# Kernel tuning notes

Hardware: AMD Instinct MI355X
Metric: run time of the kernel (lower is better)

The kernel has to match this reference:

```python
import jax, jax.numpy as jnp
import numpy as np
from jax import lax

B, C_IN, L = 512, 32, 512
E = 8
POOL = 16            # AdaptiveAvgPool1d(16)
D_IN = C_IN * L      # expert input = flattened x
D_OUT = 768          # pooler_output dim (hard-coded in module)
TAU = 1.0            # gumbel temperature
BN_EPS = 1e-5


def setup_inputs() -> dict:
    key = jax.random.key(0)
    ks = jax.random.split(key, 8)
    s = 0.02
    return {
        "x": jax.random.normal(ks[0], (B, C_IN, L), jnp.float32),
        "gumbel_u": jax.random.uniform(ks[1], (B, E), jnp.float32, 1e-6, 1.0 - 1e-6),
        "conv_w": jax.random.normal(ks[2], (64, C_IN, 3), jnp.float32) * s,
        "conv_b": jnp.zeros((64,), jnp.float32),
        "bn_gamma": jnp.ones((64 * POOL,), jnp.float32),
        "bn_beta": jnp.zeros((64 * POOL,), jnp.float32),
        "bn_mean": jnp.zeros((64 * POOL,), jnp.float32),
        "bn_var": jnp.ones((64 * POOL,), jnp.float32),
        "fc1_w": jax.random.normal(ks[3], (128, 64 * POOL), jnp.float32) * s,
        "fc1_b": jnp.zeros((128,), jnp.float32),
        "fc2_w": jax.random.normal(ks[4], (E, 128), jnp.float32) * s,
        "fc2_b": jnp.zeros((E,), jnp.float32),
        "expert_w": jax.random.normal(ks[5], (E, D_IN, D_OUT), jnp.float32) * s,
        "expert_b": jnp.zeros((E, D_OUT), jnp.float32),
    }


def _gelu(v):
    return jax.nn.gelu(v, approximate=False)  # torch nn.GELU default (erf)


def reference(x, gumbel_u, conv_w, conv_b, bn_gamma, bn_beta, bn_mean, bn_var,
              fc1_w, fc1_b, fc2_w, fc2_b, expert_w, expert_b):
    # ---- router ----
    h = lax.conv_general_dilated(x, conv_w, (1,), ((1, 1),),
                                 dimension_numbers=("NCH", "OIH", "NCH"))
    h = _gelu(h + conv_b[None, :, None])                     # [B,64,L]
    h = h.reshape(B, 64, POOL, L // POOL).mean(-1)           # adaptive avg pool -> [B,64,16]
    h = h.reshape(B, 64 * POOL)                              # flatten
    h = (h - bn_mean) * lax.rsqrt(bn_var + BN_EPS) * bn_gamma + bn_beta  # BN (eval)
    h = _gelu(h @ fc1_w.T + fc1_b)                           # dropout inactive in eval
    logits = h @ fc2_w.T + fc2_b                             # [B,E]

    # ---- soft gumbel-softmax gating (hard=False), then top-2 ----
    g = -jnp.log(-jnp.log(gumbel_u))
    routing_weights = jax.nn.softmax((logits + g) / TAU, axis=1)
    topv, topi = lax.top_k(routing_weights, 2)               # [B,2]
    w = topv / (topv.sum(axis=1, keepdims=True) + 1e-8)      # [B,2]

    # ---- dispatch/compute/combine (dense-expert stand-in: flatten + linear) ----
    xf = x.reshape(B, D_IN)
    all_out = jnp.einsum("bd,edh->beh", xf, expert_w) + expert_b[None]  # [B,E,768]
    sel = jnp.take_along_axis(all_out, topi[:, :, None], axis=1)        # [B,2,768]
    pooler_output = (sel * w[:, :, None]).sum(axis=1)                   # [B,768]
    return pooler_output
```

## Files before the change

### kernel.cpp

```cpp
#include <hip/hip_runtime.h>
#include <hip/hip_bf16.h>

#define NB 512
#define CIN 32
#define LEN 512
#define NE 8
#define NPOOL 16
#define DIN 16384
#define DOUT 768
#define HD 1024
#define F1 128

#define MT 256
#define NT 128
#define BK 32

typedef __attribute__((ext_vector_type(4))) float f32x4;
typedef __attribute__((ext_vector_type(8))) short s16x8;
typedef __attribute__((ext_vector_type(4))) unsigned int u32x4;

__device__ __forceinline__ float gelu_erf(float v) {
    return 0.5f * v * (1.0f + erff(v * 0.70710678118654752f));
}

__device__ __forceinline__ unsigned cvt_pk(float lo, float hi) {
    unsigned r;
    asm volatile("v_cvt_pk_bf16_f32 %0, %1, %2" : "=v"(r) : "v"(lo), "v"(hi));
    return r;
}

__device__ __forceinline__ unsigned short f2bf_u(float f) {
    union { float f; unsigned u; } x; x.f = f;
    unsigned r = x.u + 0x7fffu + ((x.u >> 16) & 1u);
    return (unsigned short)(r >> 16);
}

__device__ __forceinline__ void gload_lds16(const void* gptr, void* lptr) {
    __builtin_amdgcn_global_load_lds(
        (const __attribute__((address_space(1))) unsigned int*)gptr,
        (__attribute__((address_space(3))) unsigned int*)lptr,
        16, 0, 0);
}

__global__ __launch_bounds__(256) void krouter_conv(
    const float* __restrict__ x, const float* __restrict__ cw, const float* __restrict__ cb,
    const float* __restrict__ bng, const float* __restrict__ bnb,
    const float* __restrict__ bnm, const float* __restrict__ bnv,
    float* __restrict__ h, int* __restrict__ cnt, unsigned short* __restrict__ xbuf)
{
    __shared__ float xs[CIN * 264];
    int half = blockIdx.x;
    int b = blockIdx.y;
    int t = threadIdx.x;
    if (b == 0 && half == 0 && t < NE) cnt[t] = 0;

    int Lchunk0 = half * 64 - 1;
    const float* xb_ = x + (size_t)b * DIN;
    for (int idx = t; idx < CIN * 66; idx += 256) {
        int ci = idx / 66;
        int cc = idx - ci * 66;
        int gc = min(max(Lchunk0 + cc, 0), 127);
        f32x4 v = *(const f32x4*)(xb_ + ci * 512 + gc * 4);
        int byte = ci * 1056 + ((cc << 4) ^ (((cc >> 3) & 7) << 4));
        *(f32x4*)((char*)xs + byte) = v;
        if (cc >= 1 && cc <= 64) {
            int gc2 = Lchunk0 + cc;
            unsigned lo = cvt_pk(v[0], v[1]);
            unsigned hi = cvt_pk(v[2], v[3]);
            unsigned long long pk8 = ((unsigned long long)hi << 32) | lo;
            *(unsigned long long*)((char*)xbuf
                + ((size_t)b * DIN + ci * 512 + gc2 * 4) * 2) = pk8;
        }
    }
    __syncthreads();

    int p  = t & 7;
    int pg = half * 8 + p;
    int cq = t >> 3;
    int co0 = cq * 2, co1 = co0 + 1;

    float sa[32], sb[32];
    #pragma unroll
    for (int i = 0; i < 32; ++i) { sa[i] = 0.f; sb[i] = 0.f; }

    for (int ci = 0; ci < CIN; ++ci) {
        float f[40];
        #pragma unroll
        for (int u = 0; u < 10; ++u) {
            int lc = p * 8 + u;
            int byte = ci * 1056 + ((lc << 4) ^ (((lc >> 3) & 7) << 4));
            f32x4 v = *(const f32x4*)((const char*)xs + byte);
            f[4*u+0] = v[0]; f[4*u+1] = v[1]; f[4*u+2] = v[2]; f[4*u+3] = v[3];
        }
        if (pg == 0)  f[3]  = 0.f;
        if (pg == 15) f[36] = 0.f;
        float wa0 = cw[co0*96 + ci*3 + 0], wa1 = cw[co0*96 + ci*3 + 1], wa2 = cw[co0*96 + ci*3 + 2];
        float wb0 = cw[co1*96 + ci*3 + 0], wb1 = cw[co1*96 + ci*3 + 1], wb2 = cw[co1*96 + ci*3 + 2];
        #pragma unroll
        for (int i = 0; i < 32; ++i) {
            sa[i] = fmaf(f[i+3], wa0, fmaf(f[i+4], wa1, fmaf(f[i+5], wa2, sa[i])));
            sb[i] = fmaf(f[i+3], wb0, fmaf(f[i+4], wb1, fmaf(f[i+5], wb2, sb[i])));
        }
    }

    float ba = cb[co0], bbv = cb[co1];
    float ma = 0.f, mb = 0.f;
    #pragma unroll
    for (int i = 0; i < 32; ++i) { ma += gelu_erf(sa[i] + ba); mb += gelu_erf(sb[i] + bbv); }
    ma *= (1.f / 32.f); mb *= (1.f / 32.f);

    int oa = co0 * NPOOL + pg, ob = co1 * NPOOL + pg;
    float ra = (ma - bnm[oa]) * rsqrtf(bnv[oa] + 1e-5f) * bng[oa] + bnb[oa];
    float rb = (mb - bnm[ob]) * rsqrtf(bnv[ob] + 1e-5f) * bng[ob] + bnb[ob];
    h[(size_t)b * HD + oa] = ra;
    h[(size_t)b * HD + ob] = rb;
}

__global__ __launch_bounds__(256) void krouter_fc(
    const float* __restrict__ h, const float* __restrict__ f1w, const float* __restrict__ f1b,
    const float* __restrict__ f2w, const float* __restrict__ f2b,
    const float* __restrict__ gu,
    int* __restrict__ top2e, float* __restrict__ top2w,
    int* __restrict__ cnt, int* __restrict__ rowlist, float* __restrict__ roww)
{
    __shared__ float hs[4 * HD];
    __shared__ float h1s[4 * F1];
    __shared__ float lg[4 * NE];

    int bb = blockIdx.x * 4;
    int t = threadIdx.x;

    const f32x4* hg = (const f32x4*)(h + (size_t)bb * HD);
    f32x4* hs4 = (f32x4*)hs;
    #pragma unroll
    for (int u = 0; u < 4; ++u) hs4[t + 256 * u] = hg[t + 256 * u];
    __syncthreads();

    int j = t & 127;
    int pr = t >> 7;
    float acc[2] = {0.f, 0.f};
    const f32x4* w4 = (const f32x4*)(f1w + (size_t)j * HD);
    for (int k4 = 0; k4 < 256; ++k4) {
        f32x4 w = w4[k4];
        #pragma unroll
        for (int g = 0; g < 2; ++g) {
            f32x4 hv = hs4[(pr * 2 + g) * 256 + k4];
            acc[g] += w[0]*hv[0] + w[1]*hv[1] + w[2]*hv[2] + w[3]*hv[3];
        }
    }
    float bj = f1b[j];
    #pragma unroll
    for (int g = 0; g < 2; ++g) h1s[(pr * 2 + g) * F1 + j] = gelu_erf(acc[g] + bj);
    __syncthreads();

    if (t < 32) {
        int bi = t >> 3, e = t & 7;
        float s = f2b[e];
        const float* w = f2w + e * F1;
        const float* hh = h1s + bi * F1;
        #pragma unroll 8
        for (int k = 0; k < F1; ++k) s += hh[k] * w[k];
        lg[bi * NE + e] = s;
    }
    __syncthreads();

    if (t < 4) {
        int bi = t; int b = bb + bi;
        float r[NE];
        float mx = -1e30f;
        #pragma unroll
        for (int e = 0; e < NE; ++e) {
            float g = -logf(-logf(gu[b * NE + e]));
            r[e] = lg[bi * NE + e] + g;
            mx = fmaxf(mx, r[e]);
        }
        float sum = 0.f;
        #pragma unroll
        for (int e = 0; e < NE; ++e) { r[e] = expf(r[e] - mx); sum += r[e]; }
        float inv = 1.f / sum;
        #pragma unroll
        for (int e = 0; e < NE; ++e) r[e] *= inv;
        int e0 = 0; float v0 = r[0];
        #pragma unroll
        for (int e = 1; e < NE; ++e) if (r[e] > v0) { v0 = r[e]; e0 = e; }
        int e1 = -1; float v1 = -1.f;
        #pragma unroll
        for (int e = 0; e < NE; ++e) { if (e == e0) continue; if (r[e] > v1) { v1 = r[e]; e1 = e; } }
        float den = v0 + v1 + 1e-8f;
        float w0 = v0 / den, w1 = v1 / den;
        top2e[b * 2 + 0] = e0; top2e[b * 2 + 1] = e1;
        top2w[b * 2 + 0] = w0; top2w[b * 2 + 1] = w1;
        int p0 = atomicAdd(&cnt[e0], 1);
        rowlist[e0 * NB + p0] = b * 2 + 0; roww[e0 * NB + p0] = w0;
        int p1 = atomicAdd(&cnt[e1], 1);
        rowlist[e1 * NB + p1] = b * 2 + 1; roww[e1 * NB + p1] = w1;
    }
}

__global__ __launch_bounds__(512, 2) void kgemm(
    const unsigned short* __restrict__ xb, const float* __restrict__ ew,
    const int* __restrict__ cnt, const int* __restrict__ rowlist, const float* __restrict__ roww,
    unsigned short* __restrict__ ypart, int nkc, int kch)
{
    int nwg = gridDim.x;
    int cpx = nwg >> 3;
    int wg = (blockIdx.x & 7) * cpx + (blockIdx.x >> 3);
    int nt = wg % 6;
    int kc = (wg / 6) % nkc;
    int e  = wg / (6 * nkc);
    int cn = cnt[e];
    if (cn <= 0) return;

    __shared__ __align__(16) char As[3][MT * 64];
    __shared__ __align__(16) char Bs[2][NT * 64];

    int t = threadIdx.x;
    int wid = t >> 6, lane = t & 63;
    int wm = wid >> 1, wn = wid & 1;
    int g = lane >> 4;
    int NS = kch / BK;
    int k0 = kc * kch;

    int nl = t & 127, kg = t >> 7;
    const char* gpB = (const char*)ew + (size_t)e * DIN * DOUT * 4
                    + ((size_t)k0 + kg * 8) * (DOUT * 4) + (size_t)(nt * NT + nl) * 4;
    int swn = (nl ^ (nl >> 2)) & 3;
    int bwr_off = nl * 64 + ((kg ^ swn) << 4);

    int keya = ((lane >> 2) ^ (lane >> 4)) & 3;
    int aq = (lane & 3) ^ keya;
    int ldsA0 = wid * 2048, ldsA1 = wid * 2048 + 1024;

    int af_off[4], bf_off[4];
    #pragma unroll
    for (int mi = 0; mi < 4; ++mi) {
        int m = wm * 64 + mi * 16 + (lane & 15);
        af_off[mi] = m * 64 + ((g ^ ((m ^ (m >> 2)) & 3)) << 4);
    }
    #pragma unroll
    for (int ni = 0; ni < 4; ++ni) {
        int n = wn * 64 + ni * 16 + (lane & 15);
        bf_off[ni] = n * 64 + ((g ^ ((n ^ (n >> 2)) & 3)) << 4);
    }

    for (int row0 = 0; row0 < cn; row0 += MT) {
        int mloc = min(MT, cn - row0);
        bool wact = (wm * 64 < mloc);

        int r0 = wid * 32 + (lane >> 2);
        int r1 = r0 + 16;
        size_t ab0 = (size_t)(rowlist[e * NB + row0 + min(r0, mloc - 1)] >> 1) * ((size_t)DIN * 2);
        size_t ab1 = (size_t)(rowlist[e * NB + row0 + min(r1, mloc - 1)] >> 1) * ((size_t)DIN * 2);
        const char* gpA0 = (const char*)xb + ab0 + (size_t)k0 * 2 + (aq << 4);
        const char* gpA1 = (const char*)xb + ab1 + (size_t)k0 * 2 + (aq << 4);

        char* Acur = As[0]; char* Anx1 = As[1]; char* Anx2 = As[2];

        f32x4 acc[4][4];
        #pragma unroll
        for (int i = 0; i < 4; ++i)
            #pragma unroll
            for (int jj = 0; jj < 4; ++jj) acc[i][jj] = (f32x4){0.f, 0.f, 0.f, 0.f};

        float Bq0[8], Bq1[8];

        gload_lds16(gpA0, Acur + ldsA0);
        gload_lds16(gpA1, Acur + ldsA1);
        #pragma unroll
        for (int j = 0; j < 8; ++j) Bq0[j] = *(const float*)(gpB + j * (DOUT * 4));
        gload_lds16(gpA0 + BK * 2, Anx1 + ldsA0);
        gload_lds16(gpA1 + BK * 2, Anx1 + ldsA1);
        #pragma unroll
        for (int j = 0; j < 8; ++j)
            Bq1[j] = *(const float*)(gpB + (size_t)(BK * DOUT * 4) + j * (DOUT * 4));
        __builtin_amdgcn_sched_barrier(0);
        asm volatile("s_waitcnt vmcnt(10)" ::: "memory");
        __builtin_amdgcn_sched_barrier(0);
        {
            u32x4 pk;
            pk[0] = cvt_pk(Bq0[0], Bq0[1]); pk[1] = cvt_pk(Bq0[2], Bq0[3]);
            pk[2] = cvt_pk(Bq0[4], Bq0[5]); pk[3] = cvt_pk(Bq0[6], Bq0[7]);
            *(u32x4*)(Bs[0] + bwr_off) = pk;
        }
        asm volatile("s_waitcnt lgkmcnt(0)" ::: "memory");
        __builtin_amdgcn_sched_barrier(0);
        __builtin_amdgcn_s_barrier();
        __builtin_amdgcn_sched_barrier(0);

#define GSTEP(S, BLD, BCV)                                                        \
        {                                                                         \
            int s_ = (S);                                                         \
            if (s_ + 2 < NS) {                                                    \
                size_t ao = (size_t)(s_ + 2) * (BK * 2);                          \
                gload_lds16(gpA0 + ao, Anx2 + ldsA0);                             \
                gload_lds16(gpA1 + ao, Anx2 + ldsA1);                             \
                const char* bsrc = gpB + (size_t)(s_ + 2) * ((size_t)BK * DOUT * 4); \
                _Pragma("unroll")                                                 \
                for (int j = 0; j < 8; ++j)                                       \
                    BLD[j] = *(const float*)(bsrc + j * (DOUT * 4));              \
            }                                                                     \
            __builtin_amdgcn_sched_barrier(0);                                    \
            if (wact) {                                                           \
                const char* Bb = Bs[s_ & 1];                                      \
                __builtin_amdgcn_s_setprio(1);                                    \
                s16x8 af[4];                                                      \
                _Pragma("unroll")                                                 \
                for (int mi = 0; mi < 4; ++mi)                                    \
                    af[mi] = *(const s16x8*)(Acur + af_off[mi]);                  \
                _Pragma("unroll")                                                 \
                for (int ni = 0; ni < 4; ++ni) {                                  \
                    s16x8 bf = *(const s16x8*)(Bb + bf_off[ni]);                  \
                    _Pragma("unroll")                                             \
                    for (int mi = 0; mi < 4; ++mi)                                \
                        acc[mi][ni] = __builtin_amdgcn_mfma_f32_16x16x32_bf16(    \
                            af[mi], bf, acc[mi][ni], 0, 0, 0);                    \
                }                                                                 \
                __builtin_amdgcn_s_setprio(0);                                    \
            }                                                                     \
            __builtin_amdgcn_sched_barrier(0);                                    \
            if (s_ + 2 < NS)      asm volatile("s_waitcnt vmcnt(10)" ::: "memory"); \
            else if (s_ + 1 < NS) asm volatile("s_waitcnt vmcnt(0)" ::: "memory"); \
            __builtin_amdgcn_sched_barrier(0);                                    \
            if (s_ + 1 < NS) {                                                    \
                u32x4 pk;                                                         \
                pk[0] = cvt_pk(BCV[0], BCV[1]); pk[1] = cvt_pk(BCV[2], BCV[3]);   \
                pk[2] = cvt_pk(BCV[4], BCV[5]); pk[3] = cvt_pk(BCV[6], BCV[7]);   \
                *(u32x4*)(Bs[(s_ + 1) & 1] + bwr_off) = pk;                       \
            }                                                                     \
            asm volatile("s_waitcnt lgkmcnt(0)" ::: "memory");                    \
            __builtin_amdgcn_sched_barrier(0);                                    \
            __builtin_amdgcn_s_barrier();                                         \
            __builtin_amdgcn_sched_barrier(0);                                    \
            { char* tmp_ = Acur; Acur = Anx1; Anx1 = Anx2; Anx2 = tmp_; }         \
        }

        for (int s = 0; s < NS; s += 2) {
            GSTEP(s, Bq0, Bq1);
            GSTEP(s + 1, Bq1, Bq0);
        }
#undef GSTEP

        if (wact) {
            #pragma unroll
            for (int mi = 0; mi < 4; ++mi) {
                #pragma unroll
                for (int rg = 0; rg < 4; ++rg) {
                    int m = wm * 64 + mi * 16 + g * 4 + rg;
                    if (m < mloc) {
                        int ent = rowlist[e * NB + row0 + m];
                        float wgt = roww[e * NB + row0 + m];
                        int ob = ent >> 1, slot = ent & 1;
                        unsigned short* dst = ypart + ((size_t)(slot * nkc + kc) * NB + ob) * DOUT
                                            + nt * NT + wn * 64 + (lane & 15);
                        #pragma unroll
                        for (int ni = 0; ni < 4; ++ni)
                            dst[ni * 16] = f2bf_u(acc[mi][ni][rg] * wgt);
                    }
                }
            }
        }
        asm volatile("s_waitcnt vmcnt(0) lgkmcnt(0)" ::: "memory");
        __builtin_amdgcn_s_barrier();
    }
}

__global__ __launch_bounds__(256) void kcombine(
    const unsigned short* __restrict__ ypart,
    const int* __restrict__ top2e, const float* __restrict__ top2w,
    const float* __restrict__ eb, float* __restrict__ out, int nplanes)
{
    int b = blockIdx.y;
    int n = blockIdx.x * 256 + threadIdx.x;
    float s = 0.f;
    for (int p = 0; p < nplanes; ++p) {
        unsigned v = ypart[((size_t)p * NB + b) * DOUT + n];
        union { unsigned u; float f; } c; c.u = v << 16;
        s += c.f;
    }
    int e0 = top2e[b * 2], e1 = top2e[b * 2 + 1];
    float w0 = top2w[b * 2], w1 = top2w[b * 2 + 1];
    s += w0 * eb[e0 * DOUT + n] + w1 * eb[e1 * DOUT + n];
    out[(size_t)b * DOUT + n] = s;
}

extern "C" void kernel_launch(void* const* d_in, const int* in_sizes, int n_in,
                              void* d_out, int out_size, void* d_ws, size_t ws_size,
                              hipStream_t stream)
{
    const float* x   = (const float*)d_in[0];
    const float* gu  = (const float*)d_in[1];
    const float* cw  = (const float*)d_in[2];
    const float* cb  = (const float*)d_in[3];
    const float* bng = (const float*)d_in[4];
    const float* bnb = (const float*)d_in[5];
    const float* bnm = (const float*)d_in[6];
    const float* bnv = (const float*)d_in[7];
    const float* f1w = (const float*)d_in[8];
    const float* f1b = (const float*)d_in[9];
    const float* f2w = (const float*)d_in[10];
    const float* f2b = (const float*)d_in[11];
    const float* ew  = (const float*)d_in[12];
    const float* eb  = (const float*)d_in[13];

    int nkc = (ws_size >= (size_t)48 * 1024 * 1024) ? 16 : 8;
    int kch = DIN / nkc;

    char* ws = (char*)d_ws;
    size_t off = 0;
    float* h       = (float*)(ws + off); off += (size_t)NB * HD * 4;
    int*   top2e   = (int*)(ws + off);   off += (size_t)NB * 2 * 4;
    float* top2w   = (float*)(ws + off); off += (size_t)NB * 2 * 4;
    int*   cnt     = (int*)(ws + off);   off += 256;
    int*   rowlist = (int*)(ws + off);   off += (size_t)NE * NB * 4;
    float* roww    = (float*)(ws + off); off += (size_t)NE * NB * 4;
    unsigned short* xbuf = (unsigned short*)(ws + off);
    off += (size_t)NB * DIN * 2;
    unsigned short* ypart = (unsigned short*)(ws + off);
    off += (size_t)2 * nkc * NB * DOUT * 2;

    krouter_conv<<<dim3(2, NB), 256, 0, stream>>>(x, cw, cb, bng, bnb, bnm, bnv, h, cnt, xbuf);
    krouter_fc<<<NB / 4, 256, 0, stream>>>(h, f1w, f1b, f2w, f2b, gu,
                                           top2e, top2w, cnt, rowlist, roww);
    kgemm<<<NE * nkc * 6, 512, 0, stream>>>(xbuf, ew, cnt, rowlist, roww, ypart, nkc, kch);
    kcombine<<<dim3(3, NB), 256, 0, stream>>>(ypart, top2e, top2w, eb, (float*)d_out, 2 * nkc);
}
```

Measured before the change: 265.8 us.

## Replace LDS-staged expert GEMM with register-direct MFMA strips per wave

The grouped expert GEMM no longer stages A and B tiles through shared memory with barriers. Each wave now owns a 32-column output strip and loads A fragments (gathered token rows) and fp32 B weights straight into registers, converts B to bf16 in registers and issues MFMAs over 160-row M chunks with double-buffered register prefetch. The workgroup shrinks to 256 threads and the K split is fixed at 16. This removes LDS traffic and barrier synchronisation, but A rows are re-read from global memory by every strip and register pressure rises with 10 M fragments.

After: 337.1 us. 26.8% more time.

```diff
diff --git a/kernel.cpp b/kernel.cpp
--- a/kernel.cpp
+++ b/kernel.cpp
@@ -11,9 +11,10 @@
 #define HD 1024
 #define F1 128
 
-#define MT 256
-#define NT 128
 #define BK 32
+#define MFR 10
+#define KSPLIT 16
+#define NSTRIP 24
 
 typedef __attribute__((ext_vector_type(4))) float f32x4;
 typedef __attribute__((ext_vector_type(8))) short s16x8;
@@ -33,13 +34,6 @@
     union { float f; unsigned u; } x; x.f = f;
     unsigned r = x.u + 0x7fffu + ((x.u >> 16) & 1u);
     return (unsigned short)(r >> 16);
-}
-
-__device__ __forceinline__ void gload_lds16(const void* gptr, void* lptr) {
-    __builtin_amdgcn_global_load_lds(
-        (const __attribute__((address_space(1))) unsigned int*)gptr,
-        (__attribute__((address_space(3))) unsigned int*)lptr,
-        16, 0, 0);
 }
 
 __global__ __launch_bounds__(256) void krouter_conv(
@@ -197,171 +191,107 @@
     }
 }
 
-__global__ __launch_bounds__(512, 2) void kgemm(
+__global__ __launch_bounds__(256, 2) void kgemm(
     const unsigned short* __restrict__ xb, const float* __restrict__ ew,
     const int* __restrict__ cnt, const int* __restrict__ rowlist, const float* __restrict__ roww,
-    unsigned short* __restrict__ ypart, int nkc, int kch)
+    unsigned short* __restrict__ ypart, int kch)
 {
     int nwg = gridDim.x;
     int cpx = nwg >> 3;
     int wg = (blockIdx.x & 7) * cpx + (blockIdx.x >> 3);
-    int nt = wg % 6;
-    int kc = (wg / 6) % nkc;
-    int e  = wg / (6 * nkc);
-    int cn = cnt[e];
-    if (cn <= 0) return;
-
-    __shared__ __align__(16) char As[3][MT * 64];
-    __shared__ __align__(16) char Bs[2][NT * 64];
+    int e  = wg / (KSPLIT * 6);
+    int r  = wg % (KSPLIT * 6);
+    int kc = r / 6;
+    int bg = r % 6;
 
     int t = threadIdx.x;
     int wid = t >> 6, lane = t & 63;
-    int wm = wid >> 1, wn = wid & 1;
+    int st = bg * 4 + wid;
     int g = lane >> 4;
+    int cn = cnt[e];
     int NS = kch / BK;
     int k0 = kc * kch;
 
-    int nl = t & 127, kg = t >> 7;
     const char* gpB = (const char*)ew + (size_t)e * DIN * DOUT * 4
-                    + ((size_t)k0 + kg * 8) * (DOUT * 4) + (size_t)(nt * NT + nl) * 4;
-    int swn = (nl ^ (nl >> 2)) & 3;
-    int bwr_off = nl * 64 + ((kg ^ swn) << 4);
-
-    int keya = ((lane >> 2) ^ (lane >> 4)) & 3;
-    int aq = (lane & 3) ^ keya;
-    int ldsA0 = wid * 2048, ldsA1 = wid * 2048 + 1024;
-
-    int af_off[4], bf_off[4];
-    #pragma unroll
-    for (int mi = 0; mi < 4; ++mi) {
-        int m = wm * 64 + mi * 16 + (lane & 15);
-        af_off[mi] = m * 64 + ((g ^ ((m ^ (m >> 2)) & 3)) << 4);
-    }
-    #pragma unroll
-    for (int ni = 0; ni < 4; ++ni) {
-        int n = wn * 64 + ni * 16 + (lane & 15);
-        bf_off[ni] = n * 64 + ((g ^ ((n ^ (n >> 2)) & 3)) << 4);
-    }
-
-    for (int row0 = 0; row0 < cn; row0 += MT) {
-        int mloc = min(MT, cn - row0);
-        bool wact = (wm * 64 < mloc);
-
-        int r0 = wid * 32 + (lane >> 2);
-        int r1 = r0 + 16;
-        size_t ab0 = (size_t)(rowlist[e * NB + row0 + min(r0, mloc - 1)] >> 1) * ((size_t)DIN * 2);
-        size_t ab1 = (size_t)(rowlist[e * NB + row0 + min(r1, mloc - 1)] >> 1) * ((size_t)DIN * 2);
-        const char* gpA0 = (const char*)xb + ab0 + (size_t)k0 * 2 + (aq << 4);
-        const char* gpA1 = (const char*)xb + ab1 + (size_t)k0 * 2 + (aq << 4);
-
-        char* Acur = As[0]; char* Anx1 = As[1]; char* Anx2 = As[2];
-
-        f32x4 acc[4][4];
-        #pragma unroll
-        for (int i = 0; i < 4; ++i)
+                    + ((size_t)k0 + g * 8) * (DOUT * 4)
+                    + (size_t)(st * 32 + (lane & 15)) * 4;
+
+#define LOADA(AS, s_)                                                    \
+    _Pragma("unroll")                                                    \
+    for (int mi = 0; mi < MFR; ++mi)                                     \
+        AS[mi] = *(const s16x8*)(abase[mi] + (s_) * (BK * 2));
+
+#define LOADB(BS, s_) {                                                  \
+    const char* bp_ = gpB + (size_t)(s_) * ((size_t)BK * DOUT * 4);      \
+    _Pragma("unroll")                                                    \
+    for (int nf = 0; nf < 2; ++nf)                                       \
+        _Pragma("unroll")                                                \
+        for (int i = 0; i < 8; ++i)                                      \
+            BS[nf][i] = *(const float*)(bp_ + (size_t)i * (DOUT * 4) + nf * 64); }
+
+#define STEP(AC, BC, AN, BN, s_) {                                       \
+    if ((s_) + 1 < NS) { LOADA(AN, (s_) + 1); LOADB(BN, (s_) + 1); }     \
+    _Pragma("unroll")                                                    \
+    for (int nf = 0; nf < 2; ++nf) {                                     \
+        union { u32x4 u; s16x8 v8; } bf_;                                \
+        bf_.u[0] = cvt_pk(BC[nf][0], BC[nf][1]);                         \
+        bf_.u[1] = cvt_pk(BC[nf][2], BC[nf][3]);                         \
+        bf_.u[2] = cvt_pk(BC[nf][4], BC[nf][5]);                         \
+        bf_.u[3] = cvt_pk(BC[nf][6], BC[nf][7]);                         \
+        _Pragma("unroll")                                                \
+        for (int mi = 0; mi < MFR; ++mi)                                 \
+            acc[mi][nf] = __builtin_amdgcn_mfma_f32_16x16x32_bf16(       \
+                AC[mi], bf_.v8, acc[mi][nf], 0, 0, 0);                   \
+    } }
+
+    for (int row0 = 0; row0 < cn; row0 += 16 * MFR) {
+        const char* abase[MFR];
+        #pragma unroll
+        for (int mi = 0; mi < MFR; ++mi) {
+            int m = min(row0 + mi * 16 + (lane & 15), cn - 1);
+            int row = rowlist[e * NB + m] >> 1;
+            abase[mi] = (const char*)xb + (size_t)row * (DIN * 2)
+                      + (size_t)k0 * 2 + g * 16;
+        }
+
+        f32x4 acc[MFR][2];
+        #pragma unroll
+        for (int i = 0; i < MFR; ++i) {
+            acc[i][0] = (f32x4){0.f, 0.f, 0.f, 0.f};
+            acc[i][1] = (f32x4){0.f, 0.f, 0.f, 0.f};
+        }
+
+        s16x8 A0[MFR], A1[MFR];
+        float B0[2][8], B1[2][8];
+
+        LOADA(A0, 0);
+        LOADB(B0, 0);
+        for (int s = 0; s < NS; s += 2) {
+            STEP(A0, B0, A1, B1, s);
+            STEP(A1, B1, A0, B0, s + 1);
+        }
+
+        #pragma unroll
+        for (int mi = 0; mi < MFR; ++mi) {
             #pragma unroll
-            for (int jj = 0; jj < 4; ++jj) acc[i][jj] = (f32x4){0.f, 0.f, 0.f, 0.f};
-
-        float Bq0[8], Bq1[8];
-
-        gload_lds16(gpA0, Acur + ldsA0);
-        gload_lds16(gpA1, Acur + ldsA1);
-        #pragma unroll
-        for (int j = 0; j < 8; ++j) Bq0[j] = *(const float*)(gpB + j * (DOUT * 4));
-        gload_lds16(gpA0 + BK * 2, Anx1 + ldsA0);
-        gload_lds16(gpA1 + BK * 2, Anx1 + ldsA1);
-        #pragma unroll
-        for (int j = 0; j < 8; ++j)
-            Bq1[j] = *(const float*)(gpB + (size_t)(BK * DOUT * 4) + j * (DOUT * 4));
-        __builtin_amdgcn_sched_barrier(0);
-        asm volatile("s_waitcnt vmcnt(10)" ::: "memory");
-        __builtin_amdgcn_sched_barrier(0);
-        {
-            u32x4 pk;
-            pk[0] = cvt_pk(Bq0[0], Bq0[1]); pk[1] = cvt_pk(Bq0[2], Bq0[3]);
-            pk[2] = cvt_pk(Bq0[4], Bq0[5]); pk[3] = cvt_pk(Bq0[6], Bq0[7]);
-            *(u32x4*)(Bs[0] + bwr_off) = pk;
-        }
-        asm volatile("s_waitcnt lgkmcnt(0)" ::: "memory");
-        __builtin_amdgcn_sched_barrier(0);
-        __builtin_amdgcn_s_barrier();
-        __builtin_amdgcn_sched_barrier(0);
-
-#define GSTEP(S, BLD, BCV)                                                        \
-        {                                                                         \
-            int s_ = (S);                                                         \
-            if (s_ + 2 < NS) {                                                    \
-                size_t ao = (size_t)(s_ + 2) * (BK * 2);                          \
-                gload_lds16(gpA0 + ao, Anx2 + ldsA0);                             \
-                gload_lds16(gpA1 + ao, Anx2 + ldsA1);                             \
-                const char* bsrc = gpB + (size_t)(s_ + 2) * ((size_t)BK * DOUT * 4); \
-                _Pragma("unroll")                                                 \
-                for (int j = 0; j < 8; ++j)                                       \
-                    BLD[j] = *(const float*)(bsrc + j * (DOUT * 4));              \
-            }                                                                     \
-            __builtin_amdgcn_sched_barrier(0);                                    \
-            if (wact) {                                                           \
-                const char* Bb = Bs[s_ & 1];                                      \
-                __builtin_amdgcn_s_setprio(1);                                    \
-                s16x8 af[4];                                                      \
-                _Pragma("unroll")                                                 \
-                for (int mi = 0; mi < 4; ++mi)                                    \
-                    af[mi] = *(const s16x8*)(Acur + af_off[mi]);                  \
-                _Pragma("unroll")                                                 \
-                for (int ni = 0; ni < 4; ++ni) {                                  \
-                    s16x8 bf = *(const s16x8*)(Bb + bf_off[ni]);                  \
-                    _Pragma("unroll")                                             \
-                    for (int mi = 0; mi < 4; ++mi)                                \
-                        acc[mi][ni] = __builtin_amdgcn_mfma_f32_16x16x32_bf16(    \
-                            af[mi], bf, acc[mi][ni], 0, 0, 0);                    \
-                }                                                                 \
-                __builtin_amdgcn_s_setprio(0);                                    \
-            }                                                                     \
-            __builtin_amdgcn_sched_barrier(0);                                    \
-            if (s_ + 2 < NS)      asm volatile("s_waitcnt vmcnt(10)" ::: "memory"); \
-            else if (s_ + 1 < NS) asm volatile("s_waitcnt vmcnt(0)" ::: "memory"); \
-            __builtin_amdgcn_sched_barrier(0);                                    \
-            if (s_ + 1 < NS) {                                                    \
-                u32x4 pk;                                                         \
-                pk[0] = cvt_pk(BCV[0], BCV[1]); pk[1] = cvt_pk(BCV[2], BCV[3]);   \
-                pk[2] = cvt_pk(BCV[4], BCV[5]); pk[3] = cvt_pk(BCV[6], BCV[7]);   \
-                *(u32x4*)(Bs[(s_ + 1) & 1] + bwr_off) = pk;                       \
-            }                                                                     \
-            asm volatile("s_waitcnt lgkmcnt(0)" ::: "memory");                    \
-            __builtin_amdgcn_sched_barrier(0);                                    \
-            __builtin_amdgcn_s_barrier();                                         \
-            __builtin_amdgcn_sched_barrier(0);                                    \
-            { char* tmp_ = Acur; Acur = Anx1; Anx1 = Anx2; Anx2 = tmp_; }         \
-        }
-
-        for (int s = 0; s < NS; s += 2) {
-            GSTEP(s, Bq0, Bq1);
-            GSTEP(s + 1, Bq1, Bq0);
-        }
-#undef GSTEP
-
-        if (wact) {
-            #pragma unroll
-            for (int mi = 0; mi < 4; ++mi) {
-                #pragma unroll
-                for (int rg = 0; rg < 4; ++rg) {
-                    int m = wm * 64 + mi * 16 + g * 4 + rg;
-                    if (m < mloc) {
-                        int ent = rowlist[e * NB + row0 + m];
-                        float wgt = roww[e * NB + row0 + m];
-                        int ob = ent >> 1, slot = ent & 1;
-                        unsigned short* dst = ypart + ((size_t)(slot * nkc + kc) * NB + ob) * DOUT
-                                            + nt * NT + wn * 64 + (lane & 15);
-                        #pragma unroll
-                        for (int ni = 0; ni < 4; ++ni)
-                            dst[ni * 16] = f2bf_u(acc[mi][ni][rg] * wgt);
-                    }
+            for (int rg = 0; rg < 4; ++rg) {
+                int m = row0 + mi * 16 + g * 4 + rg;
+                if (m < cn) {
+                    int ent = rowlist[e * NB + m];
+                    float wgt = roww[e * NB + m];
+                    int ob = ent >> 1, slot = ent & 1;
+                    unsigned short* dst = ypart
+                        + ((size_t)(slot * KSPLIT + kc) * NB + ob) * DOUT
+                        + st * 32 + (lane & 15);
+                    dst[0]  = f2bf_u(acc[mi][0][rg] * wgt);
+                    dst[16] = f2bf_u(acc[mi][1][rg] * wgt);
                 }
             }
         }
-        asm volatile("s_waitcnt vmcnt(0) lgkmcnt(0)" ::: "memory");
-        __builtin_amdgcn_s_barrier();
-    }
+    }
+#undef LOADA
+#undef LOADB
+#undef STEP
 }
 
 __global__ __launch_bounds__(256) void kcombine(
@@ -402,8 +332,7 @@
     const float* ew  = (const float*)d_in[12];
     const float* eb  = (const float*)d_in[13];
 
-    int nkc = (ws_size >= (size_t)48 * 1024 * 1024) ? 16 : 8;
-    int kch = DIN / nkc;
+    int kch = DIN / KSPLIT;
 
     char* ws = (char*)d_ws;
     size_t off = 0;
@@ -416,11 +345,12 @@
     unsigned short* xbuf = (unsigned short*)(ws + off);
     off += (size_t)NB * DIN * 2;
     unsigned short* ypart = (unsigned short*)(ws + off);
-    off += (size_t)2 * nkc * NB * DOUT * 2;
+    off += (size_t)2 * KSPLIT * NB * DOUT * 2;
 
     krouter_conv<<<dim3(2, NB), 256, 0, stream>>>(x, cw, cb, bng, bnb, bnm, bnv, h, cnt, xbuf);
     krouter_fc<<<NB / 4, 256, 0, stream>>>(h, f1w, f1b, f2w, f2b, gu,
                                            top2e, top2w, cnt, rowlist, roww);
-    kgemm<<<NE * nkc * 6, 512, 0, stream>>>(xbuf, ew, cnt, rowlist, roww, ypart, nkc, kch);
-    kcombine<<<dim3(3, NB), 256, 0, stream>>>(ypart, top2e, top2w, eb, (float*)d_out, 2 * nkc);
-}
+    kgemm<<<NE * KSPLIT * 6, 256, 0, stream>>>(xbuf, ew, cnt, rowlist, roww, ypart, kch);
+    kcombine<<<dim3(3, NB), 256, 0, stream>>>(ypart, top2e, top2w, eb, (float*)d_out,
+                                              2 * KSPLIT);
+}
```
